# Kernel optimization log

Hardware: AMD Instinct MI355X
Metric: run time of the kernel (lower is better)

## Reference

```python
import jax, jax.numpy as jnp
import numpy as np
from jax import lax

HID, PROJ, DYN = 256, 256, 64
HW, BS, NQ = 6400, 16, 100


def setup_inputs() -> dict:
    key = jax.random.key(0)
    ks = jax.random.split(key, 10)
    p = lambda k, shape: jax.random.normal(k, shape, jnp.float32) * 0.02
    return {
        "query_feat": jax.random.normal(ks[0], (HW, BS, HID), jnp.float32),
        "support_feat": jax.random.normal(ks[1], (NQ, BS, HID), jnp.float32),
        "h": 80,
        "w": 80,
        "Wq": p(ks[2], (HID, PROJ)), "bq": jnp.zeros((PROJ,), jnp.float32),
        "Ws": p(ks[3], (HID, PROJ)), "bsp": jnp.zeros((PROJ,), jnp.float32),
        "W1": p(ks[4], (PROJ, DYN)), "b1": jnp.zeros((DYN,), jnp.float32),
        "W2": p(ks[5], (DYN, HID)), "b2": jnp.zeros((HID,), jnp.float32),
    }


def reference(query_feat, support_feat, h, w, Wq, bq, Ws, bsp, W1, b1, W2, b2):
    # query_feat: [hw, bs, c] -> [bs, hw, c]; support_feat: [nq, bs, c] -> [bs, nq, c]
    qf = jnp.transpose(query_feat, (1, 0, 2))
    sf = jnp.transpose(support_feat, (1, 0, 2))
    bsz, nq = sf.shape[0], sf.shape[1]
    hw = h * w

    fs_proj = sf @ Ws + bsp                      # [bs, nq, proj]
    fq_proj = qf @ Wq + bq                       # [bs, hw, proj]
    pattern = jnp.tanh(jax.nn.relu(fs_proj @ W1 + b1) @ W2 + b2)
    fs_feat = (pattern + 1.0) * fs_proj          # [bs, nq, proj]

    # bmm(fq, fs^T).T -> [bs, nq, hw]
    sim = jnp.einsum("bkp,bnp->bnk", fq_proj, fs_feat)
    similarity = sim.reshape(bsz, nq, h, w)

    # coordinate grid: x varies along w, y along h; flattened [hw, 2]
    gy = jnp.arange(h, dtype=jnp.float32) + 0.5
    gx = jnp.arange(w, dtype=jnp.float32) + 0.5
    X, Y = jnp.meshgrid(gx, gy, indexing="xy")  # each [h, w]
    coord = jnp.stack([X, Y], axis=-1).reshape(hw, 2)
    side = jnp.array([w, h], dtype=jnp.float32)

    sm = jax.nn.softmax(sim, axis=-1)            # [bs, nq, hw]
    proposal_for_loss = jnp.einsum("bnk,kd->bnd", sm, coord) / side

    # argmax peak -> one-hot -> 3x3 max-pool dilation (note (w,h) reshape per original)
    max_pos = jnp.argmax(sim, axis=-1)           # [bs, nq]
    max_mask = jax.nn.one_hot(max_pos, hw, dtype=jnp.float32).reshape(bsz, nq, w, h)
    local_mask = lax.reduce_window(
        max_mask, -jnp.inf, lax.max,
        window_dimensions=(1, 1, 3, 3), window_strides=(1, 1, 1, 1),
        padding=[(0, 0), (0, 0), (1, 1), (1, 1)],
    ).reshape(bsz, nq, hw)

    local_sm = sm * local_mask
    local_sm = local_sm / (jnp.sum(local_sm, axis=-1, keepdims=True) + 1e-10)
    proposals = jnp.einsum("bnk,kd->bnd", local_sm, coord) / side

    return proposal_for_loss, similarity, proposals
```

## Files before the change

kernel.cpp:

```cpp
#include <hip/hip_runtime.h>

#define HID 256
#define PROJ 256
#define DYN 64
#define HWD 6400
#define BSZ 16
#define NQ 100
#define HH 80
#define WW 80

typedef unsigned short u16;
typedef u16 u16x8 __attribute__((ext_vector_type(8)));
typedef __bf16 bf16x8 __attribute__((ext_vector_type(8)));
typedef float f32x4 __attribute__((ext_vector_type(4)));

__device__ __forceinline__ float bf2f(u16 h) {
    union { unsigned u; float f; } c; c.u = ((unsigned)h) << 16; return c.f;
}
__device__ __forceinline__ u16 f2bf(float f) {
    union { float f; unsigned u; } c; c.f = f;
    return (u16)((c.u + 0x7FFFu + ((c.u >> 16) & 1u)) >> 16);
}

__global__ __launch_bounds__(1024, 1) void kpre(
    const float* __restrict__ support,
    const float* __restrict__ Wq, const float* __restrict__ bq,
    const float* __restrict__ Ws, const float* __restrict__ bsp,
    const float* __restrict__ W1, const float* __restrict__ b1,
    const float* __restrict__ W2, const float* __restrict__ b2,
    u16* __restrict__ pack, float* __restrict__ cvec)
{
    const int c = blockIdx.x;
    const int b = blockIdx.y;
    const int t = threadIdx.x;

    __shared__ __align__(16) float sf_t[HID][8];
    __shared__ __align__(16) float part[4][8][256];
    __shared__ __align__(16) float fsp[8][PROJ];
    __shared__ __align__(16) float hidp[2][8][DYN];
    __shared__ __align__(16) float hid[8][DYN];
    __shared__ __align__(16) float fsf_t[PROJ][8];
    __shared__ float cacc[8][4];

    const int g = t >> 8;
    const int p = t & 255;

    {
        const int nl = t >> 7;
        const int i0 = (t & 127) * 2;
        const int n = c * 8 + nl;
        float v0 = 0.f, v1 = 0.f;
        if (n < NQ) {
            const float* sp = support + (size_t)n * (BSZ * HID) + (size_t)b * HID + i0;
            const float2 a = *reinterpret_cast<const float2*>(sp);
            v0 = a.x; v1 = a.y;
        }
        sf_t[i0][nl] = v0;
        sf_t[i0 + 1][nl] = v1;
    }
    __syncthreads();

    {
        float acc[8];
        #pragma unroll
        for (int n = 0; n < 8; ++n) acc[n] = 0.f;
        const int ibase = g * 64;
        float w[64];
        #pragma unroll
        for (int j = 0; j < 64; ++j)
            w[j] = Ws[(size_t)(ibase + j) * PROJ + p];
        __builtin_amdgcn_sched_barrier(0);
        #pragma unroll
        for (int j = 0; j < 64; ++j) {
            const f32x4 s0 = *reinterpret_cast<const f32x4*>(&sf_t[ibase + j][0]);
            const f32x4 s1 = *reinterpret_cast<const f32x4*>(&sf_t[ibase + j][4]);
            acc[0] += s0[0] * w[j]; acc[1] += s0[1] * w[j];
            acc[2] += s0[2] * w[j]; acc[3] += s0[3] * w[j];
            acc[4] += s1[0] * w[j]; acc[5] += s1[1] * w[j];
            acc[6] += s1[2] * w[j]; acc[7] += s1[3] * w[j];
        }
        #pragma unroll
        for (int n = 0; n < 8; ++n) part[g][n][p] = acc[n];
    }
    __syncthreads();
    {
        const int na = t >> 8;
        const float bb = bsp[p];
        #pragma unroll
        for (int k = 0; k < 2; ++k) {
            const int n = na + k * 4;
            fsp[n][p] = part[0][n][p] + part[1][n][p] + part[2][n][p] + part[3][n][p] + bb;
        }
    }
    __syncthreads();

    {
        const int ph = t >> 9;
        const int n = (t >> 6) & 7;
        const int d = t & 63;
        float a = 0.f;
        const int pb0 = ph * 128;
        #pragma unroll
        for (int pb = 0; pb < 128; pb += 64) {
            float w[64];
            #pragma unroll
            for (int j = 0; j < 64; ++j)
                w[j] = W1[(size_t)(pb0 + pb + j) * DYN + d];
            __builtin_amdgcn_sched_barrier(0);
            #pragma unroll
            for (int j = 0; j < 64; j += 4) {
                const f32x4 s = *reinterpret_cast<const f32x4*>(&fsp[n][pb0 + pb + j]);
                a += s[0] * w[j] + s[1] * w[j + 1] + s[2] * w[j + 2] + s[3] * w[j + 3];
            }
        }
        hidp[ph][n][d] = a;
    }
    __syncthreads();
    if (t < 512) {
        const int n = t >> 6, d = t & 63;
        const float a = hidp[0][n][d] + hidp[1][n][d] + b1[d];
        hid[n][d] = a > 0.f ? a : 0.f;
    }
    __syncthreads();

    {
        const int nh = t >> 8;
        const int n0 = nh * 2, n1 = nh * 2 + 1;
        const float bqv = bq[p];
        const float b2v = b2[p];
        float w[64];
        #pragma unroll
        for (int d = 0; d < 64; ++d) w[d] = W2[(size_t)d * PROJ + p];
        __builtin_amdgcn_sched_barrier(0);
        float a0 = 0.f, a1 = 0.f;
        #pragma unroll
        for (int d0 = 0; d0 < 64; d0 += 4) {
            const f32x4 h0 = *reinterpret_cast<const f32x4*>(&hid[n0][d0]);
            const f32x4 h1 = *reinterpret_cast<const f32x4*>(&hid[n1][d0]);
            a0 += h0[0] * w[d0] + h0[1] * w[d0 + 1] + h0[2] * w[d0 + 2] + h0[3] * w[d0 + 3];
            a1 += h1[0] * w[d0] + h1[1] * w[d0 + 1] + h1[2] * w[d0 + 2] + h1[3] * w[d0 + 3];
        }
        const float pat0 = tanhf(a0 + b2v);
        const float pat1 = tanhf(a1 + b2v);
        const float ff0 = (pat0 + 1.f) * fsp[n0][p];
        const float ff1 = (pat1 + 1.f) * fsp[n1][p];
        *reinterpret_cast<float2*>(&fsf_t[p][n0]) = make_float2(ff0, ff1);
        float cp0 = bqv * ff0, cp1 = bqv * ff1;
        for (int off = 32; off > 0; off >>= 1) {
            cp0 += __shfl_down(cp0, off);
            cp1 += __shfl_down(cp1, off);
        }
        const int lane = t & 63;
        const int ps = (t >> 6) & 3;
        if (lane == 0) { cacc[n0][ps] = cp0; cacc[n1][ps] = cp1; }
    }
    __syncthreads();
    if (t < 8) {
        const int n = c * 8 + t;
        if (n < NQ) cvec[b * NQ + n] = cacc[t][0] + cacc[t][1] + cacc[t][2] + cacc[t][3];
    }

    {
        const int h = p;
        float acc[8];
        #pragma unroll
        for (int n = 0; n < 8; ++n) acc[n] = 0.f;
        const int pbase = g * 64;
        f32x4 wv4[16];
        #pragma unroll
        for (int k = 0; k < 16; ++k)
            wv4[k] = *reinterpret_cast<const f32x4*>(Wq + (size_t)h * PROJ + pbase + k * 4);
        __builtin_amdgcn_sched_barrier(0);
        #pragma unroll
        for (int k = 0; k < 16; ++k) {
            #pragma unroll
            for (int m = 0; m < 4; ++m) {
                const int pp = pbase + k * 4 + m;
                const float w = wv4[k][m];
                const f32x4 f0 = *reinterpret_cast<const f32x4*>(&fsf_t[pp][0]);
                const f32x4 f1 = *reinterpret_cast<const f32x4*>(&fsf_t[pp][4]);
                acc[0] += f0[0] * w; acc[1] += f0[1] * w;
                acc[2] += f0[2] * w; acc[3] += f0[3] * w;
                acc[4] += f1[0] * w; acc[5] += f1[1] * w;
                acc[6] += f1[2] * w; acc[7] += f1[3] * w;
            }
        }
        #pragma unroll
        for (int n = 0; n < 8; ++n) part[g][n][h] = acc[n];
    }
    __syncthreads();

    {
        const int h = p;
        const int na = t >> 8;
        const int ks = h >> 5, quad = (h >> 3) & 3, j = h & 7;
        const int nt = c >> 1;
        #pragma unroll
        for (int k = 0; k < 2; ++k) {
            const int nl = na + k * 4;
            const int n = c * 8 + nl;
            float f = part[0][nl][h] + part[1][nl][h] + part[2][nl][h] + part[3][nl][h];
            if (n >= NQ) f = 0.f;
            const u16 hi = f2bf(f);
            const u16 lo = f2bf(f - bf2f(hi));
            const int nit = (c & 1) * 8 + nl;
            const int lane2 = quad * 16 + nit;
            const size_t base = ((((size_t)b * 2 + 0) * 8 + ks) * 8 + nt) * 512 + lane2 * 8 + j;
            pack[base] = hi;
            pack[base + (size_t)8 * 8 * 512] = lo;
        }
    }
}

__global__ __launch_bounds__(256, 2) void ksim(
    const float* __restrict__ qf,
    const u16* __restrict__ pack,
    const float* __restrict__ cvec,
    float* __restrict__ sim)
{
    const int mc = blockIdx.x;
    const int b  = blockIdx.y;
    const int wv = threadIdx.x >> 6;
    const int lane = threadIdx.x & 63;
    const int quad = lane >> 4, l16 = lane & 15;

    __shared__ __align__(16) u16 sbuf[2][28][512];

    const u16* pbase = pack + (size_t)b * 65536;

    #define STAGE2(KP, BUF)                                                         \
        do {                                                                        \
            _Pragma("unroll")                                                       \
            for (int i = 0; i < 7; ++i) {                                           \
                const int s28 = wv * 7 + i;                                         \
                const int s_ = s28 / 14;                                            \
                const int r_ = s28 % 14;                                            \
                const int ks_ = (KP) * 2 + r_ / 7;                                  \
                const int nt_ = r_ % 7;                                             \
                const u16* g_ = pbase + ((size_t)(s_ * 8 + ks_) * 8 + nt_) * 512    \
                                + (size_t)lane * 8;                                 \
                __builtin_amdgcn_global_load_lds(                                   \
                    (const __attribute__((address_space(1))) void*)g_,              \
                    (__attribute__((address_space(3))) void*)&sbuf[BUF][s28][0],    \
                    16, 0, 0);                                                      \
            }                                                                       \
        } while (0)

    f32x4 acc[7];
    #pragma unroll
    for (int nt = 0; nt < 7; ++nt) acc[nt] = (f32x4){0.f, 0.f, 0.f, 0.f};

    const int row = mc * 64 + wv * 16 + l16;
    const float* ap = qf + (size_t)row * (BSZ * HID) + b * HID + quad * 8;

    f32x4 af[16];
    {
        const float* p0 = ap + 0 * 32;
        const float* p1 = ap + 1 * 32;
        const float* p2 = ap + 2 * 32;
        const float* p3 = ap + 3 * 32;
        const float* p4 = ap + 4 * 32;
        const float* p5 = ap + 5 * 32;
        const float* p6 = ap + 6 * 32;
        const float* p7 = ap + 7 * 32;
        asm volatile(
            "global_load_dwordx4 %0, %16, off\n\t"
            "global_load_dwordx4 %1, %16, off offset:16\n\t"
            "global_load_dwordx4 %2, %17, off\n\t"
            "global_load_dwordx4 %3, %17, off offset:16\n\t"
            "global_load_dwordx4 %4, %18, off\n\t"
            "global_load_dwordx4 %5, %18, off offset:16\n\t"
            "global_load_dwordx4 %6, %19, off\n\t"
            "global_load_dwordx4 %7, %19, off offset:16\n\t"
            "global_load_dwordx4 %8, %20, off\n\t"
            "global_load_dwordx4 %9, %20, off offset:16\n\t"
            "global_load_dwordx4 %10, %21, off\n\t"
            "global_load_dwordx4 %11, %21, off offset:16\n\t"
            "global_load_dwordx4 %12, %22, off\n\t"
            "global_load_dwordx4 %13, %22, off offset:16\n\t"
            "global_load_dwordx4 %14, %23, off\n\t"
            "global_load_dwordx4 %15, %23, off offset:16\n\t"
            "s_waitcnt vmcnt(0)"
            : "=&v"(af[0]), "=&v"(af[1]), "=&v"(af[2]), "=&v"(af[3]),
              "=&v"(af[4]), "=&v"(af[5]), "=&v"(af[6]), "=&v"(af[7]),
              "=&v"(af[8]), "=&v"(af[9]), "=&v"(af[10]), "=&v"(af[11]),
              "=&v"(af[12]), "=&v"(af[13]), "=&v"(af[14]), "=&v"(af[15])
            : "v"(p0), "v"(p1), "v"(p2), "v"(p3),
              "v"(p4), "v"(p5), "v"(p6), "v"(p7));
    }
    STAGE2(0, 0);

    bf16x8 Ahi[8], Alo[8];
    #pragma unroll
    for (int ks = 0; ks < 8; ++ks) {
        #pragma unroll
        for (int j = 0; j < 4; ++j) {
            const float v0 = af[2 * ks][j];
            const __bf16 h0 = (__bf16)v0;
            Ahi[ks][j] = h0; Alo[ks][j] = (__bf16)(v0 - (float)h0);
            const float v1 = af[2 * ks + 1][j];
            const __bf16 h1 = (__bf16)v1;
            Ahi[ks][4 + j] = h1; Alo[ks][4 + j] = (__bf16)(v1 - (float)h1);
        }
    }
    __syncthreads();

    #define KS_COMPUTE(KS, BUF)                                                      \
    {                                                                                \
        const int kp_ = (KS) & 1;                                                    \
        u16x8 uh[7];                                                                 \
        _Pragma("unroll")                                                            \
        for (int nt = 0; nt < 7; ++nt)                                               \
            uh[nt] = *reinterpret_cast<const u16x8*>(&sbuf[BUF][kp_ * 7 + nt][lane * 8]); \
        _Pragma("unroll")                                                            \
        for (int nt = 0; nt < 7; ++nt) {                                             \
            const bf16x8 bh = __builtin_bit_cast(bf16x8, uh[nt]);                    \
            acc[nt] = __builtin_amdgcn_mfma_f32_16x16x32_bf16(Ahi[KS], bh, acc[nt], 0, 0, 0); \
            acc[nt] = __builtin_amdgcn_mfma_f32_16x16x32_bf16(Alo[KS], bh, acc[nt], 0, 0, 0); \
        }                                                                            \
        u16x8 ul[7];                                                                 \
        _Pragma("unroll")                                                            \
        for (int nt = 0; nt < 7; ++nt)                                               \
            ul[nt] = *reinterpret_cast<const u16x8*>(&sbuf[BUF][14 + kp_ * 7 + nt][lane * 8]); \
        _Pragma("unroll")                                                            \
        for (int nt = 0; nt < 7; ++nt) {                                             \
            const bf16x8 bl = __builtin_bit_cast(bf16x8, ul[nt]);                    \
            acc[nt] = __builtin_amdgcn_mfma_f32_16x16x32_bf16(Ahi[KS], bl, acc[nt], 0, 0, 0); \
        }                                                                            \
    }

    STAGE2(1, 1);
    KS_COMPUTE(0, 0)
    KS_COMPUTE(1, 0)
    __syncthreads();
    STAGE2(2, 0);
    KS_COMPUTE(2, 1)
    KS_COMPUTE(3, 1)
    __syncthreads();
    STAGE2(3, 1);
    KS_COMPUTE(4, 0)
    KS_COMPUTE(5, 0)
    __syncthreads();
    KS_COMPUTE(6, 1)
    KS_COMPUTE(7, 1)

    #undef KS_COMPUTE
    #undef STAGE2

    const int kbase = mc * 64 + wv * 16 + quad * 4;
    #pragma unroll
    for (int nt = 0; nt < 7; ++nt) {
        const int n = nt * 16 + l16;
        if (n >= NQ) continue;
        const float cadd = cvec[b * NQ + n];
        f32x4 o = acc[nt];
        o[0] += cadd; o[1] += cadd; o[2] += cadd; o[3] += cadd;
        *reinterpret_cast<f32x4*>(sim + (size_t)(b * NQ + n) * HWD + kbase) = o;
    }
}

__global__ __launch_bounds__(128, 2) void kfin(
    const float* __restrict__ sim,
    float* __restrict__ out)
{
    const int bn = blockIdx.x;
    const int w = threadIdx.x >> 6;
    const int lane = threadIdx.x & 63;
    const float* src = sim + (size_t)bn * HWD;

    __shared__ float redf[2][8];

    const int base = w ? 12 : 0;
    const int cnt  = w ? 13 : 12;

    f32x4 v[13];
    #pragma unroll
    for (int j = 0; j < 13; ++j)
        if (j < cnt)
            v[j] = *reinterpret_cast<const f32x4*>(src + (base + j) * 256 + lane * 4);
    __builtin_amdgcn_sched_barrier(0);

    float bv = -3.4e38f; int bi = 0x7FFFFFFF;
    #pragma unroll
    for (int j = 0; j < 13; ++j) {
        if (j < cnt) {
            #pragma unroll
            for (int k = 0; k < 4; ++k) {
                if (v[j][k] > bv) { bv = v[j][k]; bi = (base + j) * 256 + lane * 4 + k; }
            }
        }
    }
    #pragma unroll
    for (int m = 1; m < 64; m <<= 1) {
        const float ov = __shfl_xor(bv, m);
        const int oi = __shfl_xor(bi, m);
        if (ov > bv || (ov == bv && oi < bi)) { bv = ov; bi = oi; }
    }
    if (lane == 0) { redf[w][0] = bv; redf[w][1] = __int_as_float(bi); }
    __syncthreads();
    {
        const float v0 = redf[0][0], v1 = redf[1][0];
        const int i0 = __float_as_int(redf[0][1]), i1 = __float_as_int(redf[1][1]);
        if (v1 > v0 || (v1 == v0 && i1 < i0)) { bv = v1; bi = i1; }
        else { bv = v0; bi = i0; }
    }
    const int xc = bi % WW, yc = bi / WW;

    float s1 = 0.f, sx = 0.f, sy = 0.f;
    float wl = 0.f, wx = 0.f, wyv = 0.f;
    const int g0 = base * 256 + lane * 4;
    int x = g0 % WW, y = g0 / WW;
    #pragma unroll
    for (int j = 0; j < 13; ++j) {
        if (j < cnt) {
            #pragma unroll
            for (int k = 0; k < 4; ++k) {
                int xe = x + k, ye = y;
                if (xe >= WW) { xe -= WW; ye += 1; }
                const float e = __expf(v[j][k] - bv);
                const float fx = (float)xe + 0.5f;
                const float fy = (float)ye + 0.5f;
                s1 += e; sx += e * fx; sy += e * fy;
                const int dx = xe - xc, dy = ye - yc;
                const bool inw = (dx >= -1 && dx <= 1 && dy >= -1 && dy <= 1);
                const float ew = inw ? e : 0.f;
                wl += ew; wx += ew * fx; wyv += ew * fy;
            }
        }
        x += 16; y += 3;
        if (x >= WW) { x -= WW; y += 1; }
    }
    #pragma unroll
    for (int m = 1; m < 64; m <<= 1) {
        s1 += __shfl_xor(s1, m);
        sx += __shfl_xor(sx, m);
        sy += __shfl_xor(sy, m);
        wl += __shfl_xor(wl, m);
        wx += __shfl_xor(wx, m);
        wyv += __shfl_xor(wyv, m);
    }
    if (lane == 0) {
        redf[w][2] = s1; redf[w][3] = sx; redf[w][4] = sy;
        redf[w][5] = wl; redf[w][6] = wx; redf[w][7] = wyv;
    }
    __syncthreads();

    if (w == 0 && lane == 0) {
        const float S1 = redf[0][2] + redf[1][2];
        const float SX = redf[0][3] + redf[1][3];
        const float SY = redf[0][4] + redf[1][4];
        const float WL = redf[0][5] + redf[1][5];
        const float WX = redf[0][6] + redf[1][6];
        const float WY = redf[0][7] + redf[1][7];
        const float invS = 1.f / S1;
        out[(size_t)bn * 2 + 0] = SX * invS / (float)WW;
        out[(size_t)bn * 2 + 1] = SY * invS / (float)HH;
        const float den = WL + 1e-10f * S1;
        const size_t pbase = 3200 + (size_t)BSZ * NQ * HWD;
        out[pbase + (size_t)bn * 2 + 0] = WX / den / (float)WW;
        out[pbase + (size_t)bn * 2 + 1] = WY / den / (float)HH;
    }
}

extern "C" void kernel_launch(void* const* d_in, const int* in_sizes, int n_in,
                              void* d_out, int out_size, void* d_ws, size_t ws_size,
                              hipStream_t stream) {
    const float* qf  = (const float*)d_in[0];
    const float* sf  = (const float*)d_in[1];
    const float* Wq  = (const float*)d_in[4];
    const float* bq  = (const float*)d_in[5];
    const float* Ws  = (const float*)d_in[6];
    const float* bsp = (const float*)d_in[7];
    const float* W1  = (const float*)d_in[8];
    const float* b1  = (const float*)d_in[9];
    const float* W2  = (const float*)d_in[10];
    const float* b2  = (const float*)d_in[11];

    u16*   pack  = (u16*)d_ws;
    float* cvec  = (float*)((char*)d_ws + 2097152);
    float* out   = (float*)d_out;
    float* sim   = out + 3200;

    kpre<<<dim3(14, 16), 1024, 0, stream>>>(sf, Wq, bq, Ws, bsp, W1, b1, W2, b2, pack, cvec);
    ksim<<<dim3(100, 16), 256, 0, stream>>>(qf, pack, cvec, sim);
    kfin<<<1600, 64 * 2, 0, stream>>>(sim, out);
}
```

Before: 254.0 us.

## Fuse online-softmax partial reductions into sim GEMM epilogue, shrink final kernel

The sim GEMM epilogue now computes per-tile partial max, argmax, exp-sum and coordinate-weighted sums for each query and merges them across waves in shared memory. It writes the partials to a workspace buffer. The final kernel merges the 100 partials per row with online-softmax rescaling and re-reads only the 3x3 neighbourhood around the argmax. This replaces the full re-read of the 41MB similarity tensor. The cost is extra exp and shuffle work plus a block barrier in the GEMM epilogue, and a small workspace write.

```diff
diff --git a/kernel.cpp b/kernel.cpp
--- a/kernel.cpp
+++ b/kernel.cpp
@@ -216,7 +216,8 @@
     const float* __restrict__ qf,
     const u16* __restrict__ pack,
     const float* __restrict__ cvec,
-    float* __restrict__ sim)
+    float* __restrict__ sim,
+    float* __restrict__ gpart)
 {
     const int mc = blockIdx.x;
     const int b  = blockIdx.y;
@@ -225,6 +226,7 @@
     const int quad = lane >> 4, l16 = lane & 15;
 
     __shared__ __align__(16) u16 sbuf[2][28][512];
+    __shared__ float spart[4][7][16][5];
 
     const u16* pbase = pack + (size_t)b * 65536;
 
@@ -348,117 +350,151 @@
     #undef STAGE2
 
     const int kbase = mc * 64 + wv * 16 + quad * 4;
+    float fx4[4], fy4[4];
+    #pragma unroll
+    for (int r = 0; r < 4; ++r) {
+        const int h = kbase + r;
+        fx4[r] = (float)(h % WW) + 0.5f;
+        fy4[r] = (float)(h / WW) + 0.5f;
+    }
     #pragma unroll
     for (int nt = 0; nt < 7; ++nt) {
         const int n = nt * 16 + l16;
-        if (n >= NQ) continue;
-        const float cadd = cvec[b * NQ + n];
+        const float cadd = (n < NQ) ? cvec[b * NQ + n] : 0.f;
         f32x4 o = acc[nt];
         o[0] += cadd; o[1] += cadd; o[2] += cadd; o[3] += cadd;
-        *reinterpret_cast<f32x4*>(sim + (size_t)(b * NQ + n) * HWD + kbase) = o;
+        if (n < NQ)
+            *reinterpret_cast<f32x4*>(sim + (size_t)(b * NQ + n) * HWD + kbase) = o;
+
+        float mx = o[0]; int mi = kbase;
+        if (o[1] > mx) { mx = o[1]; mi = kbase + 1; }
+        if (o[2] > mx) { mx = o[2]; mi = kbase + 2; }
+        if (o[3] > mx) { mx = o[3]; mi = kbase + 3; }
+        #pragma unroll
+        for (int mm = 16; mm <= 32; mm <<= 1) {
+            const float ov = __shfl_xor(mx, mm);
+            const int oi = __shfl_xor(mi, mm);
+            if (ov > mx || (ov == mx && oi < mi)) { mx = ov; mi = oi; }
+        }
+        float s1 = 0.f, sx = 0.f, sy = 0.f;
+        #pragma unroll
+        for (int r = 0; r < 4; ++r) {
+            const float e = __expf(o[r] - mx);
+            s1 += e; sx += e * fx4[r]; sy += e * fy4[r];
+        }
+        #pragma unroll
+        for (int mm = 16; mm <= 32; mm <<= 1) {
+            s1 += __shfl_xor(s1, mm);
+            sx += __shfl_xor(sx, mm);
+            sy += __shfl_xor(sy, mm);
+        }
+        if (quad == 0) {
+            spart[wv][nt][l16][0] = mx;
+            spart[wv][nt][l16][1] = s1;
+            spart[wv][nt][l16][2] = sx;
+            spart[wv][nt][l16][3] = sy;
+            spart[wv][nt][l16][4] = __int_as_float(mi);
+        }
+    }
+    __syncthreads();
+
+    {
+        const int t = threadIdx.x;
+        if (t < 112) {
+            const int n = t, nt_ = t >> 4, l16_ = t & 15;
+            float M  = spart[0][nt_][l16_][0];
+            float S1 = spart[0][nt_][l16_][1];
+            float SX = spart[0][nt_][l16_][2];
+            float SY = spart[0][nt_][l16_][3];
+            int   BI = __float_as_int(spart[0][nt_][l16_][4]);
+            #pragma unroll
+            for (int w = 1; w < 4; ++w) {
+                const float m2 = spart[w][nt_][l16_][0];
+                const float s2 = spart[w][nt_][l16_][1];
+                const float x2 = spart[w][nt_][l16_][2];
+                const float y2 = spart[w][nt_][l16_][3];
+                const int  bi2 = __float_as_int(spart[w][nt_][l16_][4]);
+                const float nM = fmaxf(M, m2);
+                const float ea = __expf(M - nM), eb = __expf(m2 - nM);
+                S1 = S1 * ea + s2 * eb;
+                SX = SX * ea + x2 * eb;
+                SY = SY * ea + y2 * eb;
+                if (m2 > M || (m2 == M && bi2 < BI)) BI = bi2;
+                M = nM;
+            }
+            if (n < NQ) {
+                float* gp = gpart + ((size_t)(b * NQ + n) * 100 + mc) * 5;
+                gp[0] = M; gp[1] = S1; gp[2] = SX; gp[3] = SY;
+                gp[4] = __int_as_float(BI);
+            }
+        }
     }
 }
 
-__global__ __launch_bounds__(128, 2) void kfin(
+__global__ __launch_bounds__(64, 4) void kfin2(
     const float* __restrict__ sim,
+    const float* __restrict__ gpart,
     float* __restrict__ out)
 {
     const int bn = blockIdx.x;
-    const int w = threadIdx.x >> 6;
-    const int lane = threadIdx.x & 63;
-    const float* src = sim + (size_t)bn * HWD;
-
-    __shared__ float redf[2][8];
-
-    const int base = w ? 12 : 0;
-    const int cnt  = w ? 13 : 12;
-
-    f32x4 v[13];
+    const int lane = threadIdx.x;
+    const float* gp = gpart + (size_t)bn * 100 * 5;
+
+    float M, S1, SX, SY; int BI;
+    {
+        const float* p = gp + lane * 5;
+        M = p[0]; S1 = p[1]; SX = p[2]; SY = p[3]; BI = __float_as_int(p[4]);
+    }
+    if (lane < 36) {
+        const float* p = gp + (64 + lane) * 5;
+        const float m2 = p[0], s2 = p[1], x2 = p[2], y2 = p[3];
+        const int bi2 = __float_as_int(p[4]);
+        const float nM = fmaxf(M, m2);
+        const float ea = __expf(M - nM), eb = __expf(m2 - nM);
+        S1 = S1 * ea + s2 * eb; SX = SX * ea + x2 * eb; SY = SY * ea + y2 * eb;
+        if (m2 > M || (m2 == M && bi2 < BI)) BI = bi2;
+        M = nM;
+    }
     #pragma unroll
-    for (int j = 0; j < 13; ++j)
-        if (j < cnt)
-            v[j] = *reinterpret_cast<const f32x4*>(src + (base + j) * 256 + lane * 4);
-    __builtin_amdgcn_sched_barrier(0);
-
-    float bv = -3.4e38f; int bi = 0x7FFFFFFF;
+    for (int mm = 1; mm < 64; mm <<= 1) {
+        const float m2 = __shfl_xor(M, mm);
+        const float s2 = __shfl_xor(S1, mm);
+        const float x2 = __shfl_xor(SX, mm);
+        const float y2 = __shfl_xor(SY, mm);
+        const int bi2 = __shfl_xor(BI, mm);
+        const float nM = fmaxf(M, m2);
+        const float ea = __expf(M - nM), eb = __expf(m2 - nM);
+        S1 = S1 * ea + s2 * eb; SX = SX * ea + x2 * eb; SY = SY * ea + y2 * eb;
+        if (m2 > M || (m2 == M && bi2 < BI)) BI = bi2;
+        M = nM;
+    }
+
+    const int xc = BI % WW, yc = BI / WW;
+    float wl = 0.f, wx = 0.f, wy = 0.f;
+    if (lane < 9) {
+        const int xe = xc + (lane % 3) - 1;
+        const int ye = yc + (lane / 3) - 1;
+        if (xe >= 0 && xe < WW && ye >= 0 && ye < HH) {
+            const float v = sim[(size_t)bn * HWD + ye * WW + xe];
+            const float e = __expf(v - M);
+            wl = e; wx = e * ((float)xe + 0.5f); wy = e * ((float)ye + 0.5f);
+        }
+    }
     #pragma unroll
-    for (int j = 0; j < 13; ++j) {
-        if (j < cnt) {
-            #pragma unroll
-            for (int k = 0; k < 4; ++k) {
-                if (v[j][k] > bv) { bv = v[j][k]; bi = (base + j) * 256 + lane * 4 + k; }
-            }
-        }
-    }
-    #pragma unroll
-    for (int m = 1; m < 64; m <<= 1) {
-        const float ov = __shfl_xor(bv, m);
-        const int oi = __shfl_xor(bi, m);
-        if (ov > bv || (ov == bv && oi < bi)) { bv = ov; bi = oi; }
-    }
-    if (lane == 0) { redf[w][0] = bv; redf[w][1] = __int_as_float(bi); }
-    __syncthreads();
-    {
-        const float v0 = redf[0][0], v1 = redf[1][0];
-        const int i0 = __float_as_int(redf[0][1]), i1 = __float_as_int(redf[1][1]);
-        if (v1 > v0 || (v1 == v0 && i1 < i0)) { bv = v1; bi = i1; }
-        else { bv = v0; bi = i0; }
-    }
-    const int xc = bi % WW, yc = bi / WW;
-
-    float s1 = 0.f, sx = 0.f, sy = 0.f;
-    float wl = 0.f, wx = 0.f, wyv = 0.f;
-    const int g0 = base * 256 + lane * 4;
-    int x = g0 % WW, y = g0 / WW;
-    #pragma unroll
-    for (int j = 0; j < 13; ++j) {
-        if (j < cnt) {
-            #pragma unroll
-            for (int k = 0; k < 4; ++k) {
-                int xe = x + k, ye = y;
-                if (xe >= WW) { xe -= WW; ye += 1; }
-                const float e = __expf(v[j][k] - bv);
-                const float fx = (float)xe + 0.5f;
-                const float fy = (float)ye + 0.5f;
-                s1 += e; sx += e * fx; sy += e * fy;
-                const int dx = xe - xc, dy = ye - yc;
-                const bool inw = (dx >= -1 && dx <= 1 && dy >= -1 && dy <= 1);
-                const float ew = inw ? e : 0.f;
-                wl += ew; wx += ew * fx; wyv += ew * fy;
-            }
-        }
-        x += 16; y += 3;
-        if (x >= WW) { x -= WW; y += 1; }
-    }
-    #pragma unroll
-    for (int m = 1; m < 64; m <<= 1) {
-        s1 += __shfl_xor(s1, m);
-        sx += __shfl_xor(sx, m);
-        sy += __shfl_xor(sy, m);
-        wl += __shfl_xor(wl, m);
-        wx += __shfl_xor(wx, m);
-        wyv += __shfl_xor(wyv, m);
-    }
+    for (int mm = 1; mm < 16; mm <<= 1) {
+        wl += __shfl_xor(wl, mm);
+        wx += __shfl_xor(wx, mm);
+        wy += __shfl_xor(wy, mm);
+    }
+
     if (lane == 0) {
-        redf[w][2] = s1; redf[w][3] = sx; redf[w][4] = sy;
-        redf[w][5] = wl; redf[w][6] = wx; redf[w][7] = wyv;
-    }
-    __syncthreads();
-
-    if (w == 0 && lane == 0) {
-        const float S1 = redf[0][2] + redf[1][2];
-        const float SX = redf[0][3] + redf[1][3];
-        const float SY = redf[0][4] + redf[1][4];
-        const float WL = redf[0][5] + redf[1][5];
-        const float WX = redf[0][6] + redf[1][6];
-        const float WY = redf[0][7] + redf[1][7];
         const float invS = 1.f / S1;
         out[(size_t)bn * 2 + 0] = SX * invS / (float)WW;
         out[(size_t)bn * 2 + 1] = SY * invS / (float)HH;
-        const float den = WL + 1e-10f * S1;
+        const float den = wl + 1e-10f * S1;
         const size_t pbase = 3200 + (size_t)BSZ * NQ * HWD;
-        out[pbase + (size_t)bn * 2 + 0] = WX / den / (float)WW;
-        out[pbase + (size_t)bn * 2 + 1] = WY / den / (float)HH;
+        out[pbase + (size_t)bn * 2 + 0] = wx / den / (float)WW;
+        out[pbase + (size_t)bn * 2 + 1] = wy / den / (float)HH;
     }
 }
 
@@ -478,10 +514,11 @@
 
     u16*   pack  = (u16*)d_ws;
     float* cvec  = (float*)((char*)d_ws + 2097152);
+    float* gpart = (float*)((char*)d_ws + 2103552);
     float* out   = (float*)d_out;
     float* sim   = out + 3200;
 
     kpre<<<dim3(14, 16), 1024, 0, stream>>>(sf, Wq, bq, Ws, bsp, W1, b1, W2, b2, pack, cvec);
-    ksim<<<dim3(100, 16), 256, 0, stream>>>(qf, pack, cvec, sim);
-    kfin<<<1600, 64 * 2, 0, stream>>>(sim, out);
+    ksim<<<dim3(100, 16), 256, 0, stream>>>(qf, pack, cvec, sim, gpart);
+    kfin2<<<1600, 64, 0, stream>>>(sim, gpart, out);
 }
```

Measured after the change: 267.6 us. +5.4%, slower.
